# Kernel optimization log

Hardware: AMD Instinct MI355X
Metric: run time of the kernel (lower is better)

## Reference

```python
import jax, jax.numpy as jnp
import numpy as np

D_MODEL = 512
NUM_HEADS = 8
HEAD_DIM = D_MODEL // NUM_HEADS
SEQ_LEN = 4096
BATCH = 2
D_FF = 4 * D_MODEL
EPS = 1e-5


def _layer_norm(x, g, b):
    mu = jnp.mean(x, axis=-1, keepdims=True)
    var = jnp.var(x, axis=-1, keepdims=True)
    return (x - mu) * jax.lax.rsqrt(var + EPS) * g + b


def setup_inputs() -> dict:
    key = jax.random.key(0)
    ks = jax.random.split(key, 12)
    s = 0.02
    inp = {
        "x": jax.random.normal(ks[0], (BATCH, SEQ_LEN, D_MODEL), jnp.float32),
        # Linear weights stored as [in, out] (y = x @ W + b)
        "Wq": jax.random.normal(ks[1], (D_MODEL, D_MODEL), jnp.float32) * s,
        "bq": jnp.zeros((D_MODEL,), jnp.float32),
        "Wk": jax.random.normal(ks[2], (D_MODEL, D_MODEL), jnp.float32) * s,
        "bk": jnp.zeros((D_MODEL,), jnp.float32),
        "Wv": jax.random.normal(ks[3], (D_MODEL, D_MODEL), jnp.float32) * s,
        "bv": jnp.zeros((D_MODEL,), jnp.float32),
        "Wo": jax.random.normal(ks[4], (D_MODEL, D_MODEL), jnp.float32) * s,
        "bo": jnp.zeros((D_MODEL,), jnp.float32),
        "ln1_g": jnp.ones((D_MODEL,), jnp.float32),
        "ln1_b": jnp.zeros((D_MODEL,), jnp.float32),
        "ln2_g": jnp.ones((D_MODEL,), jnp.float32),
        "ln2_b": jnp.zeros((D_MODEL,), jnp.float32),
        "W1": jax.random.normal(ks[5], (D_MODEL, D_FF), jnp.float32) * s,
        "b1": jnp.zeros((D_FF,), jnp.float32),
        "W2": jax.random.normal(ks[6], (D_FF, D_MODEL), jnp.float32) * s,
        "b2": jnp.zeros((D_MODEL,), jnp.float32),
    }
    return inp


def reference(x, Wq, bq, Wk, bk, Wv, bv, Wo, bo, ln1_g, ln1_b, ln2_g, ln2_b, W1, b1, W2, b2):
    B, S, D = x.shape
    residual = x
    h = _layer_norm(x, ln1_g, ln1_b)
    # project and split heads: [B, H, S, Dh]
    def split_heads(t):
        return t.reshape(B, S, NUM_HEADS, HEAD_DIM).transpose(0, 2, 1, 3)
    q = split_heads(h @ Wq + bq)
    k = split_heads(h @ Wk + bk)
    v = split_heads(h @ Wv + bv)
    scores = jnp.einsum("bhqd,bhkd->bhqk", q, k) / (HEAD_DIM ** 0.5)
    attn = jax.nn.softmax(scores, axis=-1)
    out = jnp.einsum("bhqk,bhkd->bhqd", attn, v)
    out = out.transpose(0, 2, 1, 3).reshape(B, S, D)
    out = out @ Wo + bo
    x1 = residual + out
    h2 = _layer_norm(x1, ln2_g, ln2_b)
    ff = jax.nn.gelu(h2 @ W1 + b1, approximate=False) @ W2 + b2
    return x1 + ff
```

## Files before the change

kernel.cpp:

```cpp
#include <hip/hip_runtime.h>
#include <hip/hip_bf16.h>
#include <math.h>

typedef __hip_bfloat16 bf16;

#define D_MODEL 512
#define NUM_HEADS 8
#define HEAD_DIM 64
#define SEQ_LEN 4096
#define BATCH 2
#define D_FF 2048
#define TOKENS (BATCH * SEQ_LEN)
#define QKV_STRIDE 1536
#define KSPLIT 2

typedef short short4v __attribute__((ext_vector_type(4)));
typedef short short8v __attribute__((ext_vector_type(8)));
typedef float float4v __attribute__((ext_vector_type(4)));

union frag_u { short8v v8; short4v v4[2]; short s[8]; };
union pack_u { unsigned u[2]; short4v v4; };

__device__ __forceinline__ float b2f(bf16 v) { return __bfloat162float(v); }
__device__ __forceinline__ bf16 f2b(float v) { return __float2bfloat16(v); }
__device__ __forceinline__ short f2bs(float v) { bf16 t = __float2bfloat16(v); return *(short*)&t; }
__device__ __forceinline__ float exp2fast(float x) { return __builtin_amdgcn_exp2f(x); }

__device__ __forceinline__ unsigned pack_bf16(float lo, float hi) {
    unsigned a = __float_as_uint(hi) + 0x8000u;
    unsigned b = __float_as_uint(lo) + 0x8000u;
    return __builtin_amdgcn_perm(a, b, 0x07060302u);
}

#define AS1(p) ((__attribute__((address_space(1))) void*)(p))
#define AS3(p) ((__attribute__((address_space(3))) void*)(p))

__device__ __forceinline__ int self_detect(const unsigned* __restrict__ xw, int tid) {
    unsigned w = xw[tid & 63];
    unsigned e = (w >> 7) & 0xFFu;
    unsigned long long b = __ballot(e >= 110 && e <= 140);
    return __popcll(b) < 32;
}

__device__ __forceinline__ void do_tr(const void* __restrict__ src, bf16* __restrict__ dst,
                                      int K, int N, int n0, int k0, int fl, int tid,
                                      bf16 (*tile)[65]) {
    int c = tid & 63, r4 = tid >> 6;
#pragma unroll
    for (int t = 0; t < 16; t++) {
        int r = t * 4 + r4;
        size_t si = (size_t)(k0 + r) * N + n0 + c;
        float v = fl ? ((const float*)src)[si] : b2f(((const bf16*)src)[si]);
        tile[r][c] = f2b(v);
    }
    __syncthreads();
#pragma unroll
    for (int t = 0; t < 16; t++) {
        int r = t * 4 + r4;
        dst[(size_t)(n0 + r) * K + k0 + c] = tile[c][r];
    }
}

__global__ void prep_kernel(const void* x, const void* Wq, const void* Wk, const void* Wv,
                            const void* Wo, const void* W1, const void* W2,
                            const void* bq, const void* bk, const void* bv, const void* bo,
                            const void* b1, const void* b2,
                            const void* g1, const void* e1, const void* g2, const void* e2,
                            bf16* __restrict__ Wqkvt ,
                            bf16* __restrict__ W1t, bf16* __restrict__ W2t,
                            bf16* __restrict__ small, int* __restrict__ flag) {
    __shared__ bf16 tile[64][65];
    int blk = blockIdx.x, tid = threadIdx.x;
    int fl = self_detect((const unsigned*)x, tid);
    if (blk == 0 && tid == 0) flag[0] = fl;
    if (blk < 256) {
        int z = blk >> 6, tt = blk & 63;
        const void* src = (z == 0) ? Wq : (z == 1) ? Wk : (z == 2) ? Wv : Wo;
        do_tr(src, Wqkvt + (size_t)z * 512 * 512, 512, 512, (tt & 7) * 64, (tt >> 3) * 64,
              fl, tid, tile);
    } else if (blk < 512) {
        int tt = blk - 256;
        do_tr(W1, W1t, 512, 2048, (tt & 31) * 64, (tt >> 5) * 64, fl, tid, tile);
    } else if (blk < 768) {
        int tt = blk - 512;
        do_tr(W2, W2t, 2048, 512, (tt & 7) * 64, (tt >> 3) * 64, fl, tid, tile);
    } else {
        int i = (blk - 768) * 256 + tid;
        const void* src; int off;
        if (i < 512)       { src = bq; off = 0; }
        else if (i < 1024) { src = bk; off = 512; }
        else if (i < 1536) { src = bv; off = 1024; }
        else if (i < 2048) { src = bo; off = 1536; }
        else if (i < 4096) { src = b1; off = 2048; }
        else if (i < 4608) { src = b2; off = 4096; }
        else if (i < 5120) { src = g1; off = 4608; }
        else if (i < 5632) { src = e1; off = 5120; }
        else if (i < 6144) { src = g2; off = 5632; }
        else               { src = e2; off = 6144; }
        int j = i - off;
        small[i] = fl ? f2b(((const float*)src)[j]) : ((const bf16*)src)[j];
    }
}

template <int MODE>
__global__ void ln_kernel(const void* __restrict__ xv, const bf16* __restrict__ g,
                          const bf16* __restrict__ b, bf16* __restrict__ out,
                          const int* __restrict__ flag) {
    int t = blockIdx.x;
    int tid = threadIdx.x;
    int fl = (MODE == 2) ? *flag : 0;
    float v0, v1;
    if (fl) {
        const float* xr = (const float*)xv + (size_t)t * D_MODEL;
        v0 = xr[tid]; v1 = xr[tid + 256];
    } else {
        const bf16* xr = (const bf16*)xv + (size_t)t * D_MODEL;
        v0 = b2f(xr[tid]); v1 = b2f(xr[tid + 256]);
    }
    float s = v0 + v1, ss = v0 * v0 + v1 * v1;
    for (int o = 32; o > 0; o >>= 1) {
        s += __shfl_down(s, o);
        ss += __shfl_down(ss, o);
    }
    __shared__ float rs[4], rss[4], stat[2];
    int w = tid >> 6, l = tid & 63;
    if (l == 0) { rs[w] = s; rss[w] = ss; }
    __syncthreads();
    if (tid == 0) {
        float S = rs[0] + rs[1] + rs[2] + rs[3];
        float SS = rss[0] + rss[1] + rss[2] + rss[3];
        float mu = S / (float)D_MODEL;
        float var = SS / (float)D_MODEL - mu * mu;
        stat[0] = mu;
        stat[1] = rsqrtf(var + 1e-5f);
    }
    __syncthreads();
    float mu = stat[0], rstd = stat[1];
    bf16* orow = out + (size_t)t * D_MODEL;
    orow[tid]       = f2b((v0 - mu) * rstd * b2f(g[tid])       + b2f(b[tid]));
    orow[tid + 256] = f2b((v1 - mu) * rstd * b2f(g[tid + 256]) + b2f(b[tid + 256]));
}

__device__ __forceinline__ float gelu_tanh(float v) {
    float u = 0.7978845608f * (v + 0.044715f * v * v * v);
    float e2 = __expf(-2.f * u);
    return v / (1.f + e2);
}

template <int ACT>
__global__ __launch_bounds__(256) void mfma_gemm(
    const bf16* __restrict__ A, const bf16* __restrict__ Wt,
    const bf16* __restrict__ bias, bf16* __restrict__ Cout,
    int M, int N, int K) {
    __shared__ bf16 As[128 * 64];
    __shared__ bf16 Bs[128 * 64];
    int tid = threadIdx.x, wave = tid >> 6, lane = tid & 63;
    int m = lane & 15, g = lane >> 4;
    int row0 = blockIdx.y * 128, col0 = blockIdx.x * 128;
    int R0 = (wave >> 1) * 64, C0 = (wave & 1) * 64;
    float4v acc[4][4] = {};

    int srow = lane >> 3;
    int scol = (lane & 7) * 8;
    const bf16* Ab = A  + (size_t)(row0 + wave * 8 + srow) * K + scol;
    const bf16* Bb = Wt + (size_t)(col0 + wave * 8 + srow) * K + scol;

    for (int k0 = 0; k0 < K; k0 += 64) {
#pragma unroll
        for (int t = 0; t < 4; t++) {
            int rbase = t * 32 + wave * 8;
            __builtin_amdgcn_global_load_lds(AS1(Ab + (size_t)(t * 32) * K + k0),
                                             AS3(&As[rbase * 64]), 16, 0, 0);
            __builtin_amdgcn_global_load_lds(AS1(Bb + (size_t)(t * 32) * K + k0),
                                             AS3(&Bs[rbase * 64]), 16, 0, 0);
        }
        __syncthreads();
#pragma unroll
        for (int kk = 0; kk < 2; kk++) {
            short8v fa[4], fb[4];
#pragma unroll
            for (int i = 0; i < 4; i++)
                fa[i] = *(const short8v*)&As[(R0 + i * 16 + m) * 64 + kk * 32 + g * 8];
#pragma unroll
            for (int j = 0; j < 4; j++)
                fb[j] = *(const short8v*)&Bs[(C0 + j * 16 + m) * 64 + kk * 32 + g * 8];
#pragma unroll
            for (int i = 0; i < 4; i++)
#pragma unroll
                for (int j = 0; j < 4; j++)
                    acc[i][j] = __builtin_amdgcn_mfma_f32_16x16x32_bf16(fa[i], fb[j], acc[i][j], 0, 0, 0);
        }
        __syncthreads();
    }

#pragma unroll
    for (int i = 0; i < 4; i++) {
#pragma unroll
        for (int r = 0; r < 4; r++) {
            int row = row0 + R0 + i * 16 + g * 4 + r;
#pragma unroll
            for (int j = 0; j < 4; j++) {
                int col = col0 + C0 + j * 16 + m;
                float v = acc[i][j][r] + b2f(bias[col]);
                if (ACT == 1) v = gelu_tanh(v);
                Cout[(size_t)row * N + col] = f2b(v);
            }
        }
    }
}

template <int RES, int OUTMODE>
__global__ __launch_bounds__(256) void mfma_gemm64(
    const bf16* __restrict__ A, const bf16* __restrict__ Wt,
    const bf16* __restrict__ bias, const void* __restrict__ res,
    void* __restrict__ Cout, const int* __restrict__ flag, int M, int N, int K) {
    __shared__ bf16 As[128 * 64];
    __shared__ bf16 Bs[64 * 64];
    int tid = threadIdx.x, wave = tid >> 6, lane = tid & 63;
    int m = lane & 15, g = lane >> 4;
    int row0 = blockIdx.y * 128, col0 = blockIdx.x * 64;
    int R0 = wave * 32;
    int fl = (OUTMODE == 2 || RES == 3) ? *flag : 0;
    float4v acc[2][4] = {};

    int srow = lane >> 3;
    int scol = (lane & 7) * 8;
    const bf16* Ab = A  + (size_t)(row0 + wave * 8 + srow) * K + scol;
    const bf16* Bb = Wt + (size_t)(col0 + wave * 8 + srow) * K + scol;

    for (int k0 = 0; k0 < K; k0 += 64) {
#pragma unroll
        for (int t = 0; t < 4; t++) {
            __builtin_amdgcn_global_load_lds(AS1(Ab + (size_t)(t * 32) * K + k0),
                                             AS3(&As[(t * 32 + wave * 8) * 64]), 16, 0, 0);
            if (t < 2)
                __builtin_amdgcn_global_load_lds(AS1(Bb + (size_t)(t * 32) * K + k0),
                                                 AS3(&Bs[(t * 32 + wave * 8) * 64]), 16, 0, 0);
        }
        __syncthreads();
#pragma unroll
        for (int kk = 0; kk < 2; kk++) {
            short8v fa[2], fb[4];
#pragma unroll
            for (int i = 0; i < 2; i++)
                fa[i] = *(const short8v*)&As[(R0 + i * 16 + m) * 64 + kk * 32 + g * 8];
#pragma unroll
            for (int j = 0; j < 4; j++)
                fb[j] = *(const short8v*)&Bs[(j * 16 + m) * 64 + kk * 32 + g * 8];
#pragma unroll
            for (int i = 0; i < 2; i++)
#pragma unroll
                for (int j = 0; j < 4; j++)
                    acc[i][j] = __builtin_amdgcn_mfma_f32_16x16x32_bf16(fa[i], fb[j], acc[i][j], 0, 0, 0);
        }
        __syncthreads();
    }

#pragma unroll
    for (int i = 0; i < 2; i++) {
#pragma unroll
        for (int r = 0; r < 4; r++) {
            int row = row0 + R0 + i * 16 + g * 4 + r;
#pragma unroll
            for (int j = 0; j < 4; j++) {
                int col = col0 + j * 16 + m;
                float v = acc[i][j][r] + b2f(bias[col]);
                size_t idx = (size_t)row * N + col;
                if (RES == 2) v += b2f(((const bf16*)res)[idx]);
                if (RES == 3) v += fl ? ((const float*)res)[idx]
                                      : b2f(((const bf16*)res)[idx]);
                if (OUTMODE == 0) ((bf16*)Cout)[idx] = f2b(v);
                else {
                    if (fl) ((float*)Cout)[idx] = v;
                    else ((bf16*)Cout)[idx] = f2b(v);
                }
            }
        }
    }
}

__global__ void v_transpose(const bf16* __restrict__ qkv, bf16* __restrict__ Vt_g) {
    __shared__ bf16 tile[64][65];
    int s0 = blockIdx.x * 64;
    int bh = blockIdx.y;
    int b = bh >> 3, h = bh & 7;
    int c = threadIdx.x & 63, r4 = threadIdx.x >> 6;
    const bf16* src = qkv + ((size_t)b * SEQ_LEN + s0) * QKV_STRIDE + 1024 + h * 64;
#pragma unroll
    for (int t = 0; t < 16; t++) {
        int r = t * 4 + r4;
        tile[r][c] = src[(size_t)r * QKV_STRIDE + c];
    }
    __syncthreads();
    bf16* dst = Vt_g + (size_t)bh * 64 * SEQ_LEN + s0;
#pragma unroll
    for (int t = 0; t < 16; t++) {
        int r = t * 4 + r4;
        dst[(size_t)r * SEQ_LEN + c] = tile[c][r];
    }
}

__global__ __launch_bounds__(256, 4) void flash_attn(const bf16* __restrict__ Q,
                                                     const bf16* __restrict__ K,
                                                     const bf16* __restrict__ Vt_g,
                                                     bf16* __restrict__ Op,
                                                     float2* __restrict__ mlout) {
    __shared__ bf16 Ks[64][72];
    __shared__ bf16 Vt[64][68];
    __shared__ bf16 Pt[4][32][72];

    int tid = threadIdx.x;
    int wave = tid >> 6, lane = tid & 63;
    int m = lane & 15, g = lane >> 4;

    int bh = blockIdx.y;
    size_t base = (size_t)(bh >> 3) * SEQ_LEN * QKV_STRIDE + (size_t)(bh & 7) * HEAD_DIM;
    int q0w = blockIdx.x * 128 + wave * 32;

    const float qscale = 0.125f * 1.44269504f;
    short8v aQ[2][2];
#pragma unroll
    for (int mt = 0; mt < 2; mt++) {
        const bf16* qp = Q + base + (size_t)(q0w + mt * 16 + m) * QKV_STRIDE + g * 8;
#pragma unroll
        for (int c = 0; c < 2; c++) {
            frag_u u;
#pragma unroll
            for (int j = 0; j < 8; j++) u.s[j] = f2bs(b2f(qp[c * 32 + j]) * qscale);
            aQ[mt][c] = u.v8;
        }
    }

    float mrow[2] = {-1e30f, -1e30f};
    float lrow[2] = {0.f, 0.f};
    float4v oacc[2][4] = {};

    int sk = tid >> 2, sd = (tid & 3) * 16;
    int vrow = tid >> 2, vcol = (tid & 3) * 16;

    const unsigned short* Ku = (const unsigned short*)(K + base);
    const unsigned short* Vg = (const unsigned short*)Vt_g +
                               (size_t)bh * 64 * SEQ_LEN + (size_t)vrow * SEQ_LEN;

    int t0 = blockIdx.z * (64 / KSPLIT);
    int t1 = t0 + 64 / KSPLIT;

    short8v rk0, rk1, rv0, rv1;
    {
        int kt0 = t0 * 64;
        const unsigned short* kp = Ku + (size_t)(kt0 + sk) * QKV_STRIDE + sd;
        rk0 = *(const short8v*)(kp);
        rk1 = *(const short8v*)(kp + 8);
        rv0 = *(const short8v*)(Vg + kt0 + vcol);
        rv1 = *(const short8v*)(Vg + kt0 + vcol + 8);
        *(short8v*)&Ks[sk][sd]     = rk0;
        *(short8v*)&Ks[sk][sd + 8] = rk1;
        frag_u u0, u1; u0.v8 = rv0; u1.v8 = rv1;
        *(short4v*)&Vt[vrow][vcol]      = u0.v4[0];
        *(short4v*)&Vt[vrow][vcol + 4]  = u0.v4[1];
        *(short4v*)&Vt[vrow][vcol + 8]  = u1.v4[0];
        *(short4v*)&Vt[vrow][vcol + 12] = u1.v4[1];
    }
    __syncthreads();

    for (int t = t0; t < t1; t++) {
        if (t + 1 < t1) {
            int ktn = (t + 1) * 64;
            const unsigned short* kp = Ku + (size_t)(ktn + sk) * QKV_STRIDE + sd;
            rk0 = *(const short8v*)(kp);
            rk1 = *(const short8v*)(kp + 8);
            rv0 = *(const short8v*)(Vg + ktn + vcol);
            rv1 = *(const short8v*)(Vg + ktn + vcol + 8);
        }

        float4v st[2][4];
        __builtin_amdgcn_s_setprio(1);
#pragma unroll
        for (int kt = 0; kt < 4; kt++) {
            short8v bK0 = *(const short8v*)&Ks[kt * 16 + m][g * 8];
            short8v bK1 = *(const short8v*)&Ks[kt * 16 + m][32 + g * 8];
#pragma unroll
            for (int mt = 0; mt < 2; mt++) {
                float4v a = {0.f, 0.f, 0.f, 0.f};
                a = __builtin_amdgcn_mfma_f32_16x16x32_bf16(bK0, aQ[mt][0], a, 0, 0, 0);
                a = __builtin_amdgcn_mfma_f32_16x16x32_bf16(bK1, aQ[mt][1], a, 0, 0, 0);
                st[mt][kt] = a;
            }
        }
        __builtin_amdgcn_s_setprio(0);

#pragma unroll
        for (int mt = 0; mt < 2; mt++) {
            float a0 = fmaxf(fmaxf(st[mt][0][0], st[mt][0][1]),
                             fmaxf(st[mt][0][2], st[mt][0][3]));
            float a1 = fmaxf(fmaxf(st[mt][1][0], st[mt][1][1]),
                             fmaxf(st[mt][1][2], st[mt][1][3]));
            float a2 = fmaxf(fmaxf(st[mt][2][0], st[mt][2][1]),
                             fmaxf(st[mt][2][2], st[mt][2][3]));
            float a3 = fmaxf(fmaxf(st[mt][3][0], st[mt][3][1]),
                             fmaxf(st[mt][3][2], st[mt][3][3]));
            float tm = fmaxf(fmaxf(a0, a1), fmaxf(a2, a3));
            tm = fmaxf(tm, __shfl_xor(tm, 16));
            tm = fmaxf(tm, __shfl_xor(tm, 32));
            if (!__all(tm - mrow[mt] <= 8.f)) {
                float mnew = fmaxf(mrow[mt], tm);
                float alpha = exp2fast(mrow[mt] - mnew);
                mrow[mt] = mnew;
                lrow[mt] *= alpha;
#pragma unroll
                for (int dt = 0; dt < 4; dt++)
#pragma unroll
                    for (int r = 0; r < 4; r++) oacc[mt][dt][r] *= alpha;
            }
            float mcur = mrow[mt];
            float psum = 0.f;
#pragma unroll
            for (int kt = 0; kt < 4; kt++) {
                float p0 = exp2fast(st[mt][kt][0] - mcur);
                float p1 = exp2fast(st[mt][kt][1] - mcur);
                float p2 = exp2fast(st[mt][kt][2] - mcur);
                float p3 = exp2fast(st[mt][kt][3] - mcur);
                psum += (p0 + p1) + (p2 + p3);
                pack_u pp;
                pp.u[0] = pack_bf16(p0, p1);
                pp.u[1] = pack_bf16(p2, p3);
                *(short4v*)&Pt[wave][mt * 16 + m][kt * 16 + g * 4] = pp.v4;
            }
            lrow[mt] += psum;
        }

        short8v bP[2][2];
#pragma unroll
        for (int mt = 0; mt < 2; mt++)
#pragma unroll
            for (int c = 0; c < 2; c++)
                bP[mt][c] = *(const short8v*)&Pt[wave][mt * 16 + m][c * 32 + g * 8];

        __builtin_amdgcn_s_setprio(1);
#pragma unroll
        for (int dt = 0; dt < 4; dt++) {
#pragma unroll
            for (int c = 0; c < 2; c++) {
                frag_u u;
                u.v4[0] = *(const short4v*)&Vt[dt * 16 + m][c * 32 + g * 8];
                u.v4[1] = *(const short4v*)&Vt[dt * 16 + m][c * 32 + g * 8 + 4];
#pragma unroll
                for (int mt = 0; mt < 2; mt++)
                    oacc[mt][dt] = __builtin_amdgcn_mfma_f32_16x16x32_bf16(u.v8, bP[mt][c], oacc[mt][dt], 0, 0, 0);
            }
        }
        __builtin_amdgcn_s_setprio(0);

        __syncthreads();
        if (t + 1 < t1) {
            *(short8v*)&Ks[sk][sd]     = rk0;
            *(short8v*)&Ks[sk][sd + 8] = rk1;
            frag_u u0, u1; u0.v8 = rv0; u1.v8 = rv1;
            *(short4v*)&Vt[vrow][vcol]      = u0.v4[0];
            *(short4v*)&Vt[vrow][vcol + 4]  = u0.v4[1];
            *(short4v*)&Vt[vrow][vcol + 8]  = u1.v4[0];
            *(short4v*)&Vt[vrow][vcol + 12] = u1.v4[1];
        }
        __syncthreads();
    }

    size_t zoff = (size_t)blockIdx.z * NUM_HEADS * BATCH + bh;
    size_t pbase = zoff * (SEQ_LEN * (size_t)HEAD_DIM);
#pragma unroll
    for (int mt = 0; mt < 2; mt++) {
        float l = lrow[mt];
        l += __shfl_xor(l, 16);
        l += __shfl_xor(l, 32);
        int q = q0w + mt * 16 + m;
        bf16* orow = Op + pbase + (size_t)q * HEAD_DIM;
#pragma unroll
        for (int dt = 0; dt < 4; dt++) {
            pack_u oo;
            oo.u[0] = pack_bf16(oacc[mt][dt][0], oacc[mt][dt][1]);
            oo.u[1] = pack_bf16(oacc[mt][dt][2], oacc[mt][dt][3]);
            *(short4v*)&orow[dt * 16 + g * 4] = oo.v4;
        }
        if (g == 0) mlout[zoff * SEQ_LEN + q] = make_float2(mrow[mt], l);
    }
}

__global__ void attn_merge(const bf16* __restrict__ Op, const float2* __restrict__ ml,
                           bf16* __restrict__ O) {
    int i = blockIdx.x * 256 + threadIdx.x;
    int d = i & 63;
    int q = (i >> 6) & (SEQ_LEN - 1);
    int bh = i >> 18;
    const int HQ = NUM_HEADS * BATCH * SEQ_LEN;
    float2 a0 = ml[bh * SEQ_LEN + q];
    float2 a1 = ml[HQ + bh * SEQ_LEN + q];
    float M = fmaxf(a0.x, a1.x);
    float w0 = exp2fast(a0.x - M), w1 = exp2fast(a1.x - M);
    float inv = 1.f / (a0.y * w0 + a1.y * w1);
    const size_t NP = (size_t)HQ * HEAD_DIM;
    float o = (b2f(Op[i]) * w0 + b2f(Op[NP + i]) * w1) * inv;
    O[((size_t)((bh >> 3) * SEQ_LEN + q)) * D_MODEL + (bh & 7) * HEAD_DIM + d] = f2b(o);
}

extern "C" void kernel_launch(void* const* d_in, const int* in_sizes, int n_in,
                              void* d_out, int out_size, void* d_ws, size_t ws_size,
                              hipStream_t stream) {
    const void* x     = d_in[0];
    const void* Wq    = d_in[1];
    const void* bq    = d_in[2];
    const void* Wk    = d_in[3];
    const void* bk    = d_in[4];
    const void* Wv    = d_in[5];
    const void* bv    = d_in[6];
    const void* Wo    = d_in[7];
    const void* bo    = d_in[8];
    const void* ln1_g = d_in[9];
    const void* ln1_b = d_in[10];
    const void* ln2_g = d_in[11];
    const void* ln2_b = d_in[12];
    const void* W1    = d_in[13];
    const void* b1    = d_in[14];
    const void* W2    = d_in[15];
    const void* b2    = d_in[16];

    char* p = (char*)d_ws;
    int* flag = (int*)p;                      p += 256;
    size_t tok_d = (size_t)TOKENS * D_MODEL;
    char* region2 = p;                        p += 2 * tok_d * 2;
    bf16* x1b   = (bf16*)region2;
    bf16* hb    = (bf16*)(region2 + tok_d * 2);
    bf16* Opart = (bf16*)region2;
    bf16*  bigA = (bf16*)p;                   p += (size_t)TOKENS * D_FF * 2;
    bf16*  qkvb = bigA;
    bf16*  ab   = bigA + (size_t)TOKENS * QKV_STRIDE;
    bf16*  ffb  = bigA;
    bf16*  Wqkvt = (bf16*)p;                  p += (size_t)QKV_STRIDE * D_MODEL * 2;
    bf16*  Wot   = (bf16*)p;                  p += (size_t)D_MODEL * D_MODEL * 2;
    bf16*  W1t   = (bf16*)p;                  p += (size_t)D_FF * D_MODEL * 2;
    bf16*  W2t   = (bf16*)p;                  p += (size_t)D_MODEL * D_FF * 2;
    bf16*  Vtg   = (bf16*)p;                  p += (size_t)NUM_HEADS * BATCH * HEAD_DIM * SEQ_LEN * 2;
    float2* mlb  = (float2*)p;                p += (size_t)KSPLIT * NUM_HEADS * BATCH * SEQ_LEN * sizeof(float2);
    bf16*  small = (bf16*)p;                  p += 6656 * 2;
    bf16* bias_qkv = small + 0;
    bf16* bias_o   = small + 1536;
    bf16* b1b      = small + 2048;
    bf16* b2b      = small + 4096;
    bf16* g1b      = small + 4608;
    bf16* be1b     = small + 5120;
    bf16* g2b      = small + 5632;
    bf16* be2b     = small + 6144;

    prep_kernel<<<794, 256, 0, stream>>>(x, Wq, Wk, Wv, Wo, W1, W2,
                                         bq, bk, bv, bo, b1, b2,
                                         ln1_g, ln1_b, ln2_g, ln2_b,
                                         Wqkvt, W1t, W2t, small, flag);

    ln_kernel<2><<<TOKENS, 256, 0, stream>>>(x, g1b, be1b, hb, flag);

    mfma_gemm<0><<<dim3(QKV_STRIDE / 128, TOKENS / 128), 256, 0, stream>>>(
        hb, Wqkvt, bias_qkv, qkvb, TOKENS, QKV_STRIDE, D_MODEL);

    v_transpose<<<dim3(SEQ_LEN / 64, NUM_HEADS * BATCH), 256, 0, stream>>>(qkvb, Vtg);

    flash_attn<<<dim3(SEQ_LEN / 128, 16, KSPLIT), 256, 0, stream>>>(
        qkvb, qkvb + 512, Vtg, Opart, mlb);
    attn_merge<<<(NUM_HEADS * BATCH * SEQ_LEN * HEAD_DIM) / 256, 256, 0, stream>>>(
        Opart, mlb, ab);

    mfma_gemm64<3, 0><<<dim3(D_MODEL / 64, TOKENS / 128), 256, 0, stream>>>(
        ab, Wot, bias_o, x, x1b, flag, TOKENS, D_MODEL, D_MODEL);

    ln_kernel<0><<<TOKENS, 256, 0, stream>>>(x1b, g2b, be2b, hb, flag);

    mfma_gemm<1><<<dim3(D_FF / 128, TOKENS / 128), 256, 0, stream>>>(
        hb, W1t, b1b, ffb, TOKENS, D_FF, D_MODEL);

    mfma_gemm64<2, 2><<<dim3(D_MODEL / 64, TOKENS / 128), 256, 0, stream>>>(
        ffb, W2t, b2b, x1b, d_out, flag, TOKENS, D_MODEL, D_FF);
}
```

Baseline: 369.1 us.

## Fuse V transpose into QKV GEMM epilogue and swizzle workgroup order for XCDs

```diff
diff --git a/kernel.cpp b/kernel.cpp
--- a/kernel.cpp
+++ b/kernel.cpp
@@ -30,6 +30,19 @@
     unsigned a = __float_as_uint(hi) + 0x8000u;
     unsigned b = __float_as_uint(lo) + 0x8000u;
     return __builtin_amdgcn_perm(a, b, 0x07060302u);
+}
+
+__device__ __forceinline__ int3 swz_xyz() {
+    int gx = gridDim.x, gy = gridDim.y;
+    int id = blockIdx.x + gx * (blockIdx.y + gy * blockIdx.z);
+    int nwg = gx * gy * (int)gridDim.z;
+    int nid = (id & 7) * (nwg >> 3) + (id >> 3);
+    int3 r;
+    r.x = nid % gx;
+    int t = nid / gx;
+    r.y = t % gy;
+    r.z = t / gy;
+    return r;
 }
 
 #define AS1(p) ((__attribute__((address_space(1))) void*)(p))
@@ -151,12 +164,13 @@
 __global__ __launch_bounds__(256) void mfma_gemm(
     const bf16* __restrict__ A, const bf16* __restrict__ Wt,
     const bf16* __restrict__ bias, bf16* __restrict__ Cout,
-    int M, int N, int K) {
+    bf16* __restrict__ Vt_out, int M, int N, int K) {
     __shared__ bf16 As[128 * 64];
     __shared__ bf16 Bs[128 * 64];
     int tid = threadIdx.x, wave = tid >> 6, lane = tid & 63;
     int m = lane & 15, g = lane >> 4;
-    int row0 = blockIdx.y * 128, col0 = blockIdx.x * 128;
+    int3 sw = swz_xyz();
+    int row0 = sw.y * 128, col0 = sw.x * 128;
     int R0 = (wave >> 1) * 64, C0 = (wave & 1) * 64;
     float4v acc[4][4] = {};
 
@@ -191,6 +205,25 @@
                     acc[i][j] = __builtin_amdgcn_mfma_f32_16x16x32_bf16(fa[i], fb[j], acc[i][j], 0, 0, 0);
         }
         __syncthreads();
+    }
+
+    if (Vt_out != nullptr && col0 >= 1024) {
+#pragma unroll
+        for (int i = 0; i < 4; i++) {
+            int row = row0 + R0 + i * 16 + g * 4;
+            int b = row >> 12, s = row & (SEQ_LEN - 1);
+#pragma unroll
+            for (int j = 0; j < 4; j++) {
+                int col = col0 + C0 + j * 16 + m;
+                int hh = (col - 1024) >> 6, d = col & 63;
+                float bi = b2f(bias[col]);
+                pack_u oo;
+                oo.u[0] = pack_bf16(acc[i][j][0] + bi, acc[i][j][1] + bi);
+                oo.u[1] = pack_bf16(acc[i][j][2] + bi, acc[i][j][3] + bi);
+                *(short4v*)&Vt_out[((size_t)((b << 3) + hh) * 64 + d) * SEQ_LEN + s] = oo.v4;
+            }
+        }
+        return;
     }
 
 #pragma unroll
@@ -218,7 +251,8 @@
     __shared__ bf16 Bs[64 * 64];
     int tid = threadIdx.x, wave = tid >> 6, lane = tid & 63;
     int m = lane & 15, g = lane >> 4;
-    int row0 = blockIdx.y * 128, col0 = blockIdx.x * 64;
+    int3 sw = swz_xyz();
+    int row0 = sw.y * 128, col0 = sw.x * 64;
     int R0 = wave * 32;
     int fl = (OUTMODE == 2 || RES == 3) ? *flag : 0;
     float4v acc[2][4] = {};
@@ -279,43 +313,24 @@
     }
 }
 
-__global__ void v_transpose(const bf16* __restrict__ qkv, bf16* __restrict__ Vt_g) {
-    __shared__ bf16 tile[64][65];
-    int s0 = blockIdx.x * 64;
-    int bh = blockIdx.y;
-    int b = bh >> 3, h = bh & 7;
-    int c = threadIdx.x & 63, r4 = threadIdx.x >> 6;
-    const bf16* src = qkv + ((size_t)b * SEQ_LEN + s0) * QKV_STRIDE + 1024 + h * 64;
-#pragma unroll
-    for (int t = 0; t < 16; t++) {
-        int r = t * 4 + r4;
-        tile[r][c] = src[(size_t)r * QKV_STRIDE + c];
-    }
-    __syncthreads();
-    bf16* dst = Vt_g + (size_t)bh * 64 * SEQ_LEN + s0;
-#pragma unroll
-    for (int t = 0; t < 16; t++) {
-        int r = t * 4 + r4;
-        dst[(size_t)r * SEQ_LEN + c] = tile[c][r];
-    }
-}
-
+#define F3(a, b, c) fmaxf(fmaxf((a), (b)), (c))
 __global__ __launch_bounds__(256, 4) void flash_attn(const bf16* __restrict__ Q,
                                                      const bf16* __restrict__ K,
                                                      const bf16* __restrict__ Vt_g,
                                                      bf16* __restrict__ Op,
                                                      float2* __restrict__ mlout) {
     __shared__ bf16 Ks[64][72];
-    __shared__ bf16 Vt[64][68];
+    __shared__ bf16 Vt[64][72];
     __shared__ bf16 Pt[4][32][72];
 
     int tid = threadIdx.x;
     int wave = tid >> 6, lane = tid & 63;
     int m = lane & 15, g = lane >> 4;
 
-    int bh = blockIdx.y;
+    int3 sw = swz_xyz();
+    int bh = sw.y;
     size_t base = (size_t)(bh >> 3) * SEQ_LEN * QKV_STRIDE + (size_t)(bh & 7) * HEAD_DIM;
-    int q0w = blockIdx.x * 128 + wave * 32;
+    int q0w = sw.x * 128 + wave * 32;
 
     const float qscale = 0.125f * 1.44269504f;
     short8v aQ[2][2];
@@ -342,7 +357,7 @@
     const unsigned short* Vg = (const unsigned short*)Vt_g +
                                (size_t)bh * 64 * SEQ_LEN + (size_t)vrow * SEQ_LEN;
 
-    int t0 = blockIdx.z * (64 / KSPLIT);
+    int t0 = sw.z * (64 / KSPLIT);
     int t1 = t0 + 64 / KSPLIT;
 
     short8v rk0, rk1, rv0, rv1;
@@ -355,11 +370,8 @@
         rv1 = *(const short8v*)(Vg + kt0 + vcol + 8);
         *(short8v*)&Ks[sk][sd]     = rk0;
         *(short8v*)&Ks[sk][sd + 8] = rk1;
-        frag_u u0, u1; u0.v8 = rv0; u1.v8 = rv1;
-        *(short4v*)&Vt[vrow][vcol]      = u0.v4[0];
-        *(short4v*)&Vt[vrow][vcol + 4]  = u0.v4[1];
-        *(short4v*)&Vt[vrow][vcol + 8]  = u1.v4[0];
-        *(short4v*)&Vt[vrow][vcol + 12] = u1.v4[1];
+        *(short8v*)&Vt[vrow][vcol]     = rv0;
+        *(short8v*)&Vt[vrow][vcol + 8] = rv1;
     }
     __syncthreads();
 
@@ -391,15 +403,12 @@
 
 #pragma unroll
         for (int mt = 0; mt < 2; mt++) {
-            float a0 = fmaxf(fmaxf(st[mt][0][0], st[mt][0][1]),
-                             fmaxf(st[mt][0][2], st[mt][0][3]));
-            float a1 = fmaxf(fmaxf(st[mt][1][0], st[mt][1][1]),
-                             fmaxf(st[mt][1][2], st[mt][1][3]));
-            float a2 = fmaxf(fmaxf(st[mt][2][0], st[mt][2][1]),
-                             fmaxf(st[mt][2][2], st[mt][2][3]));
-            float a3 = fmaxf(fmaxf(st[mt][3][0], st[mt][3][1]),
-                             fmaxf(st[mt][3][2], st[mt][3][3]));
-            float tm = fmaxf(fmaxf(a0, a1), fmaxf(a2, a3));
+            float u0 = F3(st[mt][0][0], st[mt][0][1], st[mt][0][2]);
+            float u1 = F3(st[mt][0][3], st[mt][1][0], st[mt][1][1]);
+            float u2 = F3(st[mt][1][2], st[mt][1][3], st[mt][2][0]);
+            float u3 = F3(st[mt][2][1], st[mt][2][2], st[mt][2][3]);
+            float u4 = F3(st[mt][3][0], st[mt][3][1], st[mt][3][2]);
+            float tm = fmaxf(F3(u0, u1, u2), F3(u3, u4, st[mt][3][3]));
             tm = fmaxf(tm, __shfl_xor(tm, 16));
             tm = fmaxf(tm, __shfl_xor(tm, 32));
             if (!__all(tm - mrow[mt] <= 8.f)) {
@@ -441,12 +450,10 @@
         for (int dt = 0; dt < 4; dt++) {
 #pragma unroll
             for (int c = 0; c < 2; c++) {
-                frag_u u;
-                u.v4[0] = *(const short4v*)&Vt[dt * 16 + m][c * 32 + g * 8];
-                u.v4[1] = *(const short4v*)&Vt[dt * 16 + m][c * 32 + g * 8 + 4];
+                short8v av = *(const short8v*)&Vt[dt * 16 + m][c * 32 + g * 8];
 #pragma unroll
                 for (int mt = 0; mt < 2; mt++)
-                    oacc[mt][dt] = __builtin_amdgcn_mfma_f32_16x16x32_bf16(u.v8, bP[mt][c], oacc[mt][dt], 0, 0, 0);
+                    oacc[mt][dt] = __builtin_amdgcn_mfma_f32_16x16x32_bf16(av, bP[mt][c], oacc[mt][dt], 0, 0, 0);
             }
         }
         __builtin_amdgcn_s_setprio(0);
@@ -455,16 +462,13 @@
         if (t + 1 < t1) {
             *(short8v*)&Ks[sk][sd]     = rk0;
             *(short8v*)&Ks[sk][sd + 8] = rk1;
-            frag_u u0, u1; u0.v8 = rv0; u1.v8 = rv1;
-            *(short4v*)&Vt[vrow][vcol]      = u0.v4[0];
-            *(short4v*)&Vt[vrow][vcol + 4]  = u0.v4[1];
-            *(short4v*)&Vt[vrow][vcol + 8]  = u1.v4[0];
-            *(short4v*)&Vt[vrow][vcol + 12] = u1.v4[1];
+            *(short8v*)&Vt[vrow][vcol]     = rv0;
+            *(short8v*)&Vt[vrow][vcol + 8] = rv1;
         }
         __syncthreads();
     }
 
-    size_t zoff = (size_t)blockIdx.z * NUM_HEADS * BATCH + bh;
+    size_t zoff = (size_t)sw.z * NUM_HEADS * BATCH + bh;
     size_t pbase = zoff * (SEQ_LEN * (size_t)HEAD_DIM);
 #pragma unroll
     for (int mt = 0; mt < 2; mt++) {
@@ -557,9 +561,7 @@
     ln_kernel<2><<<TOKENS, 256, 0, stream>>>(x, g1b, be1b, hb, flag);
 
     mfma_gemm<0><<<dim3(QKV_STRIDE / 128, TOKENS / 128), 256, 0, stream>>>(
-        hb, Wqkvt, bias_qkv, qkvb, TOKENS, QKV_STRIDE, D_MODEL);
-
-    v_transpose<<<dim3(SEQ_LEN / 64, NUM_HEADS * BATCH), 256, 0, stream>>>(qkvb, Vtg);
+        hb, Wqkvt, bias_qkv, qkvb, Vtg, TOKENS, QKV_STRIDE, D_MODEL);
 
     flash_attn<<<dim3(SEQ_LEN / 128, 16, KSPLIT), 256, 0, stream>>>(
         qkvb, qkvb + 512, Vtg, Opart, mlb);
@@ -572,7 +574,7 @@
     ln_kernel<0><<<TOKENS, 256, 0, stream>>>(x1b, g2b, be2b, hb, flag);
 
     mfma_gemm<1><<<dim3(D_FF / 128, TOKENS / 128), 256, 0, stream>>>(
-        hb, W1t, b1b, ffb, TOKENS, D_FF, D_MODEL);
+        hb, W1t, b1b, ffb, nullptr, TOKENS, D_FF, D_MODEL);
 
     mfma_gemm64<2, 2><<<dim3(D_MODEL / 64, TOKENS / 128), 256, 0, stream>>>(
         ffb, W2t, b2b, x1b, d_out, flag, TOKENS, D_MODEL, D_FF);
```

New measurement: 355.3 us. 3.7% less time.
